# Kernel optimization log

Measured on AMD Instinct MI355X. Metric: run time of the kernel, lower is better.

Reference implementation:

```python
import jax, jax.numpy as jnp
import numpy as np

B, N, F, T, K, O = 8, 1024, 64, 32, 3, 64


def setup_inputs() -> dict:
    key = jax.random.key(0)
    k0, k1, k2, k3 = jax.random.split(key, 4)
    x = jax.random.normal(k0, (B, N, F, T), dtype=jnp.float32)
    spatial_attention = jax.random.uniform(k1, (B, N, N), dtype=jnp.float32)
    cheb = jax.random.normal(k2, (K, N, N), dtype=jnp.float32) * 0.1  # stacked T_k
    Theta = jax.random.normal(k3, (K, F, O), dtype=jnp.float32) * (1.0 / np.sqrt(F))
    return {"x": x, "spatial_attention": spatial_attention, "cheb": cheb, "Theta": Theta}


def reference(x, spatial_attention, cheb, Theta):
    # Original per-timestep, per-k loop computes:
    #   rhs[b,i,f] = sum_j (T_k[j,i] * att[b,j,i])... note: T_k_with_at.permute(0,2,1) @ x
    #   i.e. rhs[b,i,f,t] = sum_j T_k[j,i]*att[b,j,i]*x[b,j,f,t]
    # Vectorized over all timesteps t and Chebyshev orders k at once.
    rhs = jnp.einsum('kji,bji,bjft->bkift', cheb, spatial_attention, x)  # (B,K,N,F,T)
    out = jnp.einsum('bkift,kfo->biot', rhs, Theta)                      # sum over k,f
    return jax.nn.relu(out)  # (B,N,O,T)
```

## Files before the change

kernel.cpp:

```cpp
#include <hip/hip_runtime.h>
#include <stdint.h>

#define Bn 8
#define Nn 1024
#define Fn 64
#define Tn 32
#define Kn 3
#define On 64
#define Rn (Kn * Nn)
#define Cn (On * Tn)
#define NT (Rn / 64)

typedef __bf16 bf16x8 __attribute__((ext_vector_type(8)));
typedef float f32x4 __attribute__((ext_vector_type(4)));
typedef __attribute__((address_space(1))) void gvoid;
typedef __attribute__((address_space(3))) void lvoid;

union BF8 { bf16x8 v; ushort s[8]; uint4 q; };

static __device__ __forceinline__ ushort f2bf(float f) {
  uint32_t u = __float_as_uint(f);
  return (ushort)((u + 0x7FFFu + ((u >> 16) & 1u)) >> 16);
}

static __device__ __forceinline__ void glds(const ushort* g, ushort* l) {
  __builtin_amdgcn_global_load_lds((gvoid*)g, (lvoid*)l, 16, 0, 0);
}

__global__ void k_thetaT(const float* __restrict__ Theta, ushort* __restrict__ ThT) {
  int idx = blockIdx.x * 256 + threadIdx.x;
  if (idx < Kn * On * Fn) {
    int k = idx / (On * Fn);
    int rem = idx % (On * Fn);
    int o = rem / Fn, f = rem % Fn;
    ThT[idx] = f2bf(Theta[(k * Fn + f) * On + o]);
  }
}

__global__ __launch_bounds__(256) void k_prepW(const float* __restrict__ att,
                                               const float* __restrict__ cheb,
                                               ushort* __restrict__ Wt) {
  __shared__ float tile[32][33];
  int i0 = blockIdx.x * 32, j0 = blockIdx.y * 32;
  int tid = threadIdx.x;
  int ci = tid & 31, rj = tid >> 5;
  float cv[4][Kn];
#pragma unroll
  for (int p = 0; p < 4; p++) {
    int j = j0 + rj + p * 8;
#pragma unroll
    for (int k = 0; k < Kn; k++)
      cv[p][k] = cheb[((size_t)k * Nn + j) * Nn + i0 + ci];
  }
  for (int b = 0; b < Bn; b++) {
    float av[4];
#pragma unroll
    for (int p = 0; p < 4; p++) {
      int j = j0 + rj + p * 8;
      av[p] = att[((size_t)b * Nn + j) * Nn + i0 + ci];
    }
    for (int k = 0; k < Kn; k++) {
#pragma unroll
      for (int p = 0; p < 4; p++)
        tile[rj + p * 8][ci] = av[p] * cv[p][k];
      __syncthreads();
#pragma unroll
      for (int p = 0; p < 4; p++) {
        int i = i0 + rj + p * 8;
        Wt[((size_t)b * Nn + i) * Rn + (size_t)k * Nn + j0 + ci] = f2bf(tile[ci][rj + p * 8]);
      }
      __syncthreads();
    }
  }
}

__global__ __launch_bounds__(512) void k_prepY(const float* __restrict__ x,
                                               const ushort* __restrict__ ThT,
                                               ushort* __restrict__ Yt) {
  __shared__ ushort ylds[1024 * 32];
  int jt = blockIdx.x, b = blockIdx.y;
  int j0 = jt * 32;
  int tid = threadIdx.x;
  int lane = tid & 63, w = tid >> 6;
  int l15 = lane & 15, l4 = lane >> 4;

  BF8 bfr[4][2][2];
#pragma unroll
  for (int jj = 0; jj < 4; jj++) {
    const float* xp = x + ((size_t)b * Nn + (j0 + w * 4 + jj)) * (Fn * Tn);
#pragma unroll
    for (int ks = 0; ks < 2; ks++)
#pragma unroll
      for (int tf = 0; tf < 2; tf++) {
        int t = tf * 16 + l15;
        int fb = ks * 32 + l4 * 8;
#pragma unroll
        for (int e = 0; e < 8; e++)
          bfr[jj][ks][tf].s[e] = f2bf(xp[(fb + e) * Tn + t]);
      }
  }

  for (int k = 0; k < Kn; k++) {
    for (int h = 0; h < 2; h++) {
      BF8 afr[2][2];
#pragma unroll
      for (int o2 = 0; o2 < 2; o2++)
#pragma unroll
        for (int ks = 0; ks < 2; ks++) {
          int o = h * 32 + o2 * 16 + l15;
          afr[o2][ks].q = *(const uint4*)&ThT[((size_t)k * On + o) * Fn + ks * 32 + l4 * 8];
        }
#pragma unroll
      for (int jj = 0; jj < 4; jj++) {
        f32x4 acc[2][2] = {};
#pragma unroll
        for (int ks = 0; ks < 2; ks++)
#pragma unroll
          for (int o2 = 0; o2 < 2; o2++)
#pragma unroll
            for (int tf = 0; tf < 2; tf++)
              acc[o2][tf] = __builtin_amdgcn_mfma_f32_16x16x32_bf16(
                  afr[o2][ks].v, bfr[jj][ks][tf].v, acc[o2][tf], 0, 0, 0);
#pragma unroll
        for (int o2 = 0; o2 < 2; o2++)
#pragma unroll
          for (int tf = 0; tf < 2; tf++)
#pragma unroll
            for (int q = 0; q < 4; q++) {
              int cl = (o2 * 16 + l4 * 4 + q) * Tn + tf * 16 + l15;
              ylds[cl * 32 + w * 4 + jj] = f2bf(acc[o2][tf][q]);
            }
      }
      __syncthreads();
      const uint32_t* yl32 = (const uint32_t*)ylds;
      uint32_t* Yt32 = (uint32_t*)Yt;
      int e = tid & 15, rowst = tid >> 4;
      for (int pass = 0; pass < 32; pass++) {
        int cl = pass * 32 + rowst;
        size_t off = ((size_t)b * Cn + (size_t)(h * 1024 + cl)) * Rn + (size_t)k * Nn + j0;
        Yt32[off / 2 + e] = yl32[cl * 16 + e];
      }
      __syncthreads();
    }
  }
}

__global__ __launch_bounds__(512, 2) void k_gemm(const ushort* __restrict__ Wt,
                                                 const ushort* __restrict__ Yt,
                                                 float* __restrict__ out) {
  extern __shared__ __align__(16) ushort smem[];
  ushort* As = smem;
  ushort* Bs = smem + 32768;

  int g = blockIdx.x;
  int b = g & 7, slot = g >> 3;
  int i0 = (slot & 3) * 256, c0 = (slot >> 2) * 256;
  int tid = threadIdx.x, lane = tid & 63, w = tid >> 6;
  int l15 = lane & 15, l4 = lane >> 4;
  int wm = w >> 2, wn = w & 3;

  const ushort* Ab = Wt + ((size_t)b * Nn + i0) * Rn;
  const ushort* Bb = Yt + ((size_t)b * Cn + c0) * Rn;

  int srcC = (((lane & 7) ^ (lane >> 3)) * 8);
  int arow0 = w * 8 + (lane >> 3);
  int brow0 = (w >> 2) * 64 + (w & 3) * 8 + (lane >> 3);

  int aL = (wm * 64 + l15) * 64;
  int bL = (wn * 32 + l15) * 64;
  int x7 = l15 & 7;
  int colx0 = ((l4) ^ x7) * 8;
  int colx1 = ((4 + l4) ^ x7) * 8;

  f32x4 acc[8][4] = {};
  BF8 af[4][2], bf[4][2];

#define MFMA_(a_, b_, c_) __builtin_amdgcn_mfma_f32_16x16x32_bf16((a_), (b_), (c_), 0, 0, 0)
#define BAR() asm volatile("s_barrier" ::: "memory")
#define PRIO1 __builtin_amdgcn_s_setprio(1)
#define PRIO0 __builtin_amdgcn_s_setprio(0)

#define STAGE_A(t_, h_) { int bo_ = ((t_) & 1) * 16384 + (h_) * 8192 + w * 512; \
    const ushort* gp_ = Ab + (size_t)(arow0 + (h_) * 64) * Rn + (t_) * 64 + srcC; \
    glds(gp_, As + bo_); \
    glds(gp_ + 128 * (size_t)Rn, As + bo_ + 4096); }
#define STAGE_B(t_, h_) { int bo_ = ((t_) & 1) * 16384 + (h_) * 8192 + w * 512; \
    const ushort* gp_ = Bb + (size_t)(brow0 + (h_) * 32) * Rn + (t_) * 64 + srcC; \
    glds(gp_, Bs + bo_); \
    glds(gp_ + 128 * (size_t)Rn, Bs + bo_ + 4096); }

#define RD_A(mh_) { _Pragma("unroll") for (int m = 0; m < 4; m++) { \
    int ba_ = bufo + (mh_) * 8192 + aL + m * 1024; \
    af[m][0].q = *(const uint4*)&As[ba_ + colx0]; \
    af[m][1].q = *(const uint4*)&As[ba_ + colx1]; } }
#define RD_B(nh_) { _Pragma("unroll") for (int n = 0; n < 2; n++) { \
    int bb_ = bufo + (nh_) * 8192 + bL + n * 1024; \
    bf[(nh_) * 2 + n][0].q = *(const uint4*)&Bs[bb_ + colx0]; \
    bf[(nh_) * 2 + n][1].q = *(const uint4*)&Bs[bb_ + colx1]; } }
#define MM(mh_, nh_) { _Pragma("unroll") for (int ks = 0; ks < 2; ks++) \
    _Pragma("unroll") for (int m = 0; m < 4; m++) \
      _Pragma("unroll") for (int n = 0; n < 2; n++) { \
        int gm_ = (mh_) * 4 + m, gn_ = (nh_) * 2 + n; \
        acc[gm_][gn_] = MFMA_(af[m][ks].v, bf[gn_][ks].v, acc[gm_][gn_]); } }

#define VMC(n_) asm volatile("s_waitcnt vmcnt(" #n_ ")" ::: "memory")

  STAGE_A(0, 0); STAGE_B(0, 0); STAGE_B(0, 1); STAGE_A(0, 1); STAGE_A(1, 0);
  VMC(6);
  BAR();

#define TILE(t_, S1_, S2_, W0_, W1_, W3_, LAST_) { \
    int bufo = ((t_) & 1) * 16384; \
     \
    RD_A(0); RD_B(0); \
    if (S1_) STAGE_B((t_) + 1, 0); \
    BAR(); \
    PRIO1; MM(0, 0); PRIO0; \
    VMC(W0_); BAR(); \
     \
    RD_B(1); \
    if (S1_) { STAGE_B((t_) + 1, 1); STAGE_A((t_) + 1, 1); } \
    BAR(); \
    PRIO1; MM(0, 1); PRIO0; \
    VMC(W1_); BAR(); \
     \
    RD_A(1); \
    if (S2_) STAGE_A((t_) + 2, 0); \
    BAR(); \
    PRIO1; MM(1, 0); PRIO0; \
    BAR(); \
     \
    PRIO1; MM(1, 1); PRIO0; \
    if (!(LAST_)) { VMC(W3_); BAR(); } \
  }

  for (int t = 0; t < NT - 2; ++t)
    TILE(t, 1, 1, 6, 8, 6, 0);
  TILE(NT - 2, 1, 0, 6, 8, 4, 0);
  TILE(NT - 1, 0, 0, 2, 0, 0, 1);

#undef TILE
#undef VMC
#undef MM
#undef RD_B
#undef RD_A
#undef STAGE_B
#undef STAGE_A

  float* ob = out + (size_t)b * Nn * Cn;
#pragma unroll
  for (int m = 0; m < 8; m++) {
    int i = i0 + wm * 128 + m * 16 + l4 * 4;
#pragma unroll
    for (int n = 0; n < 4; n++) {
      int c = c0 + wn * 64 + n * 16 + l15;
#pragma unroll
      for (int q = 0; q < 4; q++)
        ob[(size_t)(i + q) * Cn + c] = fmaxf(acc[m][n][q], 0.0f);
    }
  }
}

extern "C" void kernel_launch(void* const* d_in, const int* in_sizes, int n_in,
                              void* d_out, int out_size, void* d_ws, size_t ws_size,
                              hipStream_t stream) {
  const float* x     = (const float*)d_in[0];
  const float* att   = (const float*)d_in[1];
  const float* cheb  = (const float*)d_in[2];
  const float* Theta = (const float*)d_in[3];
  float* out = (float*)d_out;

  char* ws = (char*)d_ws;
  ushort* ThT = (ushort*)ws;
  ushort* Wt  = (ushort*)(ws + 65536);
  ushort* Yt  = (ushort*)(ws + 65536 + 50331648ull);

  hipFuncSetAttribute((const void*)k_gemm, hipFuncAttributeMaxDynamicSharedMemorySize, 131072);

  k_thetaT<<<48, 256, 0, stream>>>(Theta, ThT);
  k_prepW<<<dim3(32, 32), 256, 0, stream>>>(att, cheb, Wt);
  k_prepY<<<dim3(32, 8), 512, 0, stream>>>(x, ThT, Yt);
  k_gemm<<<256, 512, 131072, stream>>>(Wt, Yt, out);
}
```

Before: 173.8 us.

## Double-buffer LDS fragment registers to overlap reads with MFMA quadrants

Splits the A/B fragment registers into two register sets. LDS reads for the next quadrant, and for the first quadrant of the next k-tile, are now issued before the current quadrant's MFMAs. The per-tile barrier count drops from six to three, with the vmcnt thresholds adjusted to match. This aims to hide LDS read latency behind matrix math, at the cost of higher VGPR pressure and a more delicate barrier and wait ordering across the double-buffered LDS stages.

```diff
diff --git a/kernel.cpp b/kernel.cpp
--- a/kernel.cpp
+++ b/kernel.cpp
@@ -173,12 +173,14 @@
   int colx1 = ((4 + l4) ^ x7) * 8;
 
   f32x4 acc[8][4] = {};
-  BF8 af[4][2], bf[4][2];
+  BF8 afX[4][2], afY[4][2];
+  BF8 bfX[2][2], bfY[2][2];
 
 #define MFMA_(a_, b_, c_) __builtin_amdgcn_mfma_f32_16x16x32_bf16((a_), (b_), (c_), 0, 0, 0)
 #define BAR() asm volatile("s_barrier" ::: "memory")
 #define PRIO1 __builtin_amdgcn_s_setprio(1)
 #define PRIO0 __builtin_amdgcn_s_setprio(0)
+#define VMC(n_) asm volatile("s_waitcnt vmcnt(" #n_ ")" ::: "memory")
 
 #define STAGE_A(t_, h_) { int bo_ = ((t_) & 1) * 16384 + (h_) * 8192 + w * 512; \
     const ushort* gp_ = Ab + (size_t)(arow0 + (h_) * 64) * Rn + (t_) * 64 + srcC; \
@@ -189,63 +191,53 @@
     glds(gp_, Bs + bo_); \
     glds(gp_ + 128 * (size_t)Rn, Bs + bo_ + 4096); }
 
-#define RD_A(mh_) { _Pragma("unroll") for (int m = 0; m < 4; m++) { \
-    int ba_ = bufo + (mh_) * 8192 + aL + m * 1024; \
-    af[m][0].q = *(const uint4*)&As[ba_ + colx0]; \
-    af[m][1].q = *(const uint4*)&As[ba_ + colx1]; } }
-#define RD_B(nh_) { _Pragma("unroll") for (int n = 0; n < 2; n++) { \
-    int bb_ = bufo + (nh_) * 8192 + bL + n * 1024; \
-    bf[(nh_) * 2 + n][0].q = *(const uint4*)&Bs[bb_ + colx0]; \
-    bf[(nh_) * 2 + n][1].q = *(const uint4*)&Bs[bb_ + colx1]; } }
-#define MM(mh_, nh_) { _Pragma("unroll") for (int ks = 0; ks < 2; ks++) \
+#define RD_A(DST_, bo_, mh_) { _Pragma("unroll") for (int m = 0; m < 4; m++) { \
+    int ba_ = (bo_) + (mh_) * 8192 + aL + m * 1024; \
+    DST_[m][0].q = *(const uint4*)&As[ba_ + colx0]; \
+    DST_[m][1].q = *(const uint4*)&As[ba_ + colx1]; } }
+#define RD_B(DST_, bo_, nh_) { _Pragma("unroll") for (int n = 0; n < 2; n++) { \
+    int bb_ = (bo_) + (nh_) * 8192 + bL + n * 1024; \
+    DST_[n][0].q = *(const uint4*)&Bs[bb_ + colx0]; \
+    DST_[n][1].q = *(const uint4*)&Bs[bb_ + colx1]; } }
+
+#define MMC(AF_, BF_, MO_, NO_) { _Pragma("unroll") for (int ks = 0; ks < 2; ks++) \
     _Pragma("unroll") for (int m = 0; m < 4; m++) \
-      _Pragma("unroll") for (int n = 0; n < 2; n++) { \
-        int gm_ = (mh_) * 4 + m, gn_ = (nh_) * 2 + n; \
-        acc[gm_][gn_] = MFMA_(af[m][ks].v, bf[gn_][ks].v, acc[gm_][gn_]); } }
-
-#define VMC(n_) asm volatile("s_waitcnt vmcnt(" #n_ ")" ::: "memory")
+      _Pragma("unroll") for (int n = 0; n < 2; n++) \
+        acc[(MO_) + m][(NO_) + n] = MFMA_(AF_[m][ks].v, BF_[n][ks].v, acc[(MO_) + m][(NO_) + n]); }
 
   STAGE_A(0, 0); STAGE_B(0, 0); STAGE_B(0, 1); STAGE_A(0, 1); STAGE_A(1, 0);
-  VMC(6);
-  BAR();
-
-#define TILE(t_, S1_, S2_, W0_, W1_, W3_, LAST_) { \
-    int bufo = ((t_) & 1) * 16384; \
-     \
-    RD_A(0); RD_B(0); \
-    if (S1_) STAGE_B((t_) + 1, 0); \
-    BAR(); \
-    PRIO1; MM(0, 0); PRIO0; \
+  VMC(6); BAR();
+  RD_A(afX, 0, 0); RD_B(bfX, 0, 0);
+
+#define TILE(t_, S0_, S1_, S2_, W0_, W1_, W3_, LAST_) { \
+    int bo_c = ((t_) & 1) * 16384; \
     VMC(W0_); BAR(); \
-     \
-    RD_B(1); \
+    RD_B(bfY, bo_c, 1); \
+    if (S0_) STAGE_B((t_) + 1, 0); \
+    PRIO1; MMC(afX, bfX, 0, 0); PRIO0; \
+    VMC(W1_); BAR(); \
+    RD_A(afY, bo_c, 1); \
     if (S1_) { STAGE_B((t_) + 1, 1); STAGE_A((t_) + 1, 1); } \
-    BAR(); \
-    PRIO1; MM(0, 1); PRIO0; \
-    VMC(W1_); BAR(); \
-     \
-    RD_A(1); \
+    PRIO1; MMC(afX, bfY, 0, 2); PRIO0; \
     if (S2_) STAGE_A((t_) + 2, 0); \
-    BAR(); \
-    PRIO1; MM(1, 0); PRIO0; \
-    BAR(); \
-     \
-    PRIO1; MM(1, 1); PRIO0; \
-    if (!(LAST_)) { VMC(W3_); BAR(); } \
+    PRIO1; MMC(afY, bfX, 4, 0); PRIO0; \
+    if (!(LAST_)) { VMC(W3_); BAR(); \
+      RD_A(afX, bo_c ^ 16384, 0); RD_B(bfX, bo_c ^ 16384, 0); } \
+    PRIO1; MMC(afY, bfY, 4, 2); PRIO0; \
   }
 
   for (int t = 0; t < NT - 2; ++t)
-    TILE(t, 1, 1, 6, 8, 6, 0);
-  TILE(NT - 2, 1, 0, 6, 8, 4, 0);
-  TILE(NT - 1, 0, 0, 2, 0, 0, 1);
+    TILE(t, 1, 1, 1, 4, 4, 6, 0);
+  TILE(NT - 2, 1, 1, 0, 4, 4, 4, 0);
+  TILE(NT - 1, 0, 0, 0, 2, 0, 0, 1);
 
 #undef TILE
-#undef VMC
-#undef MM
+#undef MMC
 #undef RD_B
 #undef RD_A
 #undef STAGE_B
 #undef STAGE_A
+#undef VMC
 
   float* ob = out + (size_t)b * Nn * Cn;
 #pragma unroll
```

Result: faster. 155.6 us (-10.5%).
